# Kernel optimization log

Hardware: AMD Instinct MI355X
Metric: run time of the kernel (lower is better)

The kernel has to match this reference:

```python
import jax, jax.numpy as jnp
import numpy as np
import math

B, N, M, C, H = 4, 2048, 2048, 512, 4
D_V = C // H          # 128, used for scale and value head dim
D_QK = 2 * C // H     # 256, q/k head dim due to seq-axis split of the 2*dim qkv output
SCALE = D_V ** -0.5
EPS = 1e-12           # F.normalize eps


def _l2norm(t):
    n = jnp.linalg.norm(t, axis=-1, keepdims=True)
    return t / jnp.maximum(n, EPS)


def setup_inputs() -> dict:
    key = jax.random.key(0)
    k1, k2, k3, k4 = jax.random.split(key, 4)
    x = jax.random.normal(k1, (B, N, C), dtype=jnp.float32)
    context = jax.random.normal(k2, (B, M, C), dtype=jnp.float32)
    W_qkv = jax.random.normal(k3, (2 * C, C), dtype=jnp.float32) * 0.02  # torch Linear weight [out,in]
    W_proj = jax.random.normal(k4, (C, C), dtype=jnp.float32) * 0.02
    radius = jnp.ones((H,), dtype=jnp.float32) * math.sqrt(D_V)
    return {"x": x, "context": context, "W_qkv": W_qkv, "W_proj": W_proj, "radius": radius}


def reference(x, context, W_qkv, W_proj, radius):
    # qkv(cat([x, context], dim=1)) then split along sequence: q from x rows, k from context rows
    q = jnp.einsum('bnc,oc->bno', x, W_qkv)        # [B,N,2C]
    k = jnp.einsum('bmc,oc->bmo', context, W_qkv)  # [B,M,2C]
    q = q.reshape(B, N, H, D_QK).transpose(0, 2, 1, 3)       # [B,H,N,256]
    k = k.reshape(B, M, H, D_QK).transpose(0, 2, 1, 3)       # [B,H,M,256]
    v = context.reshape(B, M, H, D_V).transpose(0, 2, 1, 3)  # [B,H,M,128]
    r = radius[None, :, None, None]
    q = _l2norm(q) * r
    k = _l2norm(k) * r
    attn = jnp.einsum('bhnd,bhmd->bhnm', q, k) * SCALE
    attn = jax.nn.softmax(attn, axis=-1)
    out = jnp.einsum('bhnm,bhmd->bhnd', attn, v)
    out = out.transpose(0, 2, 1, 3).reshape(B, N, C)
    return jnp.einsum('bnc,oc->bno', out, W_proj)
```

## Files before the change

### kernel.cpp

```cpp
#include <hip/hip_runtime.h>
#include <hip/hip_bf16.h>
#include <stdint.h>

#define SCALE_F 0.08838834764831845f

typedef __attribute__((ext_vector_type(8))) short short8;
typedef __attribute__((ext_vector_type(4))) float f32x4;
typedef __attribute__((ext_vector_type(16))) float f32x16;

__device__ __forceinline__ void g2l16(const void* g, void* l) {
  __builtin_amdgcn_global_load_lds(
      (const __attribute__((address_space(1))) void*)g,
      (__attribute__((address_space(3))) void*)l, 16, 0, 0);
}

__global__ __launch_bounds__(256) void convert_all(
    const float* __restrict__ x, const float* __restrict__ ctx,
    const float* __restrict__ wqkv, const float* __restrict__ wproj,
    __hip_bfloat16* __restrict__ ab, __hip_bfloat16* __restrict__ wb,
    __hip_bfloat16* __restrict__ wpb)
{
  size_t qi = (size_t)blockIdx.x * 256 + threadIdx.x;
  const float* src; __hip_bfloat16* dst; size_t off;
  if (qi < 1048576)      { src = x;     dst = ab;           off = qi; }
  else if (qi < 2097152) { src = ctx;   dst = ab + 4194304; off = qi - 1048576; }
  else if (qi < 2228224) { src = wqkv;  dst = wb;           off = qi - 2097152; }
  else                   { src = wproj; dst = wpb;          off = qi - 2228224; }
  float4 v = ((const float4*)src)[off];
  union { __hip_bfloat16 h4[4]; uint2 u; } o;
  o.h4[0] = __float2bfloat16(v.x); o.h4[1] = __float2bfloat16(v.y);
  o.h4[2] = __float2bfloat16(v.z); o.h4[3] = __float2bfloat16(v.w);
  ((uint2*)dst)[off] = o.u;
}

__global__ __launch_bounds__(256) void transpose_v(
    const float* __restrict__ ctx, __hip_bfloat16* __restrict__ vt)
{
  __shared__ float tile[128][33];
  const int bid = blockIdx.x;
  const int mt = bid & 63;
  const int bh = bid >> 6;
  const int h = bh & 3, b = bh >> 2;
  const int tid = threadIdx.x;
  for (int i = 0; i < 16; ++i) {
    int idx = i * 256 + tid;
    int mm = idx >> 7, d = idx & 127;
    tile[d][mm] = ctx[((size_t)b * 2048 + mt * 32 + mm) * 512 + h * 128 + d];
  }
  __syncthreads();
  for (int i = 0; i < 16; ++i) {
    int idx = i * 256 + tid;
    int d = idx >> 5, mm = idx & 31;
    vt[((size_t)bh * 128 + d) * 2048 + mt * 32 + mm] = __float2bfloat16(tile[d][mm]);
  }
}

__global__ __launch_bounds__(256) void gemm_nt(
    const __hip_bfloat16* __restrict__ A, const __hip_bfloat16* __restrict__ B,
    float* __restrict__ C, int O, int K, int tiles_o)
{
  __shared__ __hip_bfloat16 sA[128 * 32];
  __shared__ __hip_bfloat16 sB[128 * 32];
  const int tid = threadIdx.x;
  const int wave = tid >> 6, lane = tid & 63;
  const int ln = lane & 15, q = lane >> 4;
  const int br = (blockIdx.x / tiles_o) * 128;
  const int bo = (blockIdx.x % tiles_o) * 128;
  const int wr = (wave >> 1) * 64, wc = (wave & 1) * 64;
  const __hip_bfloat16* Ab = A + (size_t)br * K;
  const __hip_bfloat16* Bb = B + (size_t)bo * K;
  const int row0 = tid >> 2, p0 = tid & 3;
  f32x4 acc[4][4] = {};
  for (int k0 = 0; k0 < K; k0 += 32) {
    for (int i = 0; i < 2; ++i) {
      int row = i * 64 + row0;
      g2l16(Ab + (size_t)row * K + k0 + p0 * 8, (char*)sA + (i * 256 + tid) * 16);
      g2l16(Bb + (size_t)row * K + k0 + p0 * 8, (char*)sB + (i * 256 + tid) * 16);
    }
    __syncthreads();
    short8 af[4], bfr[4];
    for (int mi = 0; mi < 4; ++mi)
      af[mi] = *(const short8*)(sA + (wr + mi * 16 + ln) * 32 + q * 8);
    for (int ni = 0; ni < 4; ++ni)
      bfr[ni] = *(const short8*)(sB + (wc + ni * 16 + ln) * 32 + q * 8);
    for (int mi = 0; mi < 4; ++mi)
      for (int ni = 0; ni < 4; ++ni)
        acc[mi][ni] = __builtin_amdgcn_mfma_f32_16x16x32_bf16(af[mi], bfr[ni], acc[mi][ni], 0, 0, 0);
    __syncthreads();
  }
  for (int mi = 0; mi < 4; ++mi)
    for (int ni = 0; ni < 4; ++ni) {
      int rg = br + wr + mi * 16 + q * 4;
      int cg = bo + wc + ni * 16 + ln;
      for (int r = 0; r < 4; ++r)
        C[(size_t)(rg + r) * O + cg] = acc[mi][ni][r];
    }
}

__global__ __launch_bounds__(256) void normalize_qk(
    const float* __restrict__ proj, const float* __restrict__ radius,
    __hip_bfloat16* __restrict__ qn, __hip_bfloat16* __restrict__ kn)
{
  const int r = blockIdx.x;
  const int h = threadIdx.x >> 6, lane = threadIdx.x & 63;
  float4 v = *(const float4*)(proj + (size_t)r * 1024 + h * 256 + lane * 4);
  float ss = v.x * v.x + v.y * v.y + v.z * v.z + v.w * v.w;
  for (int off = 1; off < 64; off <<= 1) ss += __shfl_xor(ss, off);
  float nrm = fmaxf(sqrtf(ss), 1e-12f);
  const bool isq = r < 8192;
  const int rr = isq ? r : r - 8192;
  const float rad = radius[h];
  const float sc = (isq ? rad * rad * SCALE_F : 1.0f) / nrm;
  __hip_bfloat16* dst = (isq ? qn : kn) +
      ((size_t)((rr >> 11) * 4 + h) * 2048 + (rr & 2047)) * 256 + lane * 4;
  union { __hip_bfloat16 h4[4]; uint2 u; } o;
  o.h4[0] = __float2bfloat16(v.x * sc);
  o.h4[1] = __float2bfloat16(v.y * sc);
  o.h4[2] = __float2bfloat16(v.z * sc);
  o.h4[3] = __float2bfloat16(v.w * sc);
  *(uint2*)dst = o.u;
}

__global__ __launch_bounds__(256, 2) void attn(
    const __hip_bfloat16* __restrict__ qn,
    const __hip_bfloat16* __restrict__ kn,
    const __hip_bfloat16* __restrict__ vt,
    float* __restrict__ Op,
    float* __restrict__ den)
{
  __shared__ __hip_bfloat16 sK[2][32 * 256];
  __shared__ __hip_bfloat16 sV[2][128 * 32];
  __shared__ __hip_bfloat16 sP[4][32 * 40];
  const int tid = threadIdx.x, wave = tid >> 6, lane = tid & 63;
  const int m32 = lane & 31, hi = lane >> 5;
  const int i = blockIdx.x;
  const int bh = (i & 7) + 8 * ((i >> 3) & 1);
  const int half = (i >> 4) & 1;
  const int nt = i >> 5;
  const int mbase = half * 1024;
  const __hip_bfloat16* Q = qn + ((size_t)bh * 2048 + nt * 128 + wave * 32) * 256;
  const __hip_bfloat16* Kp = kn + (size_t)bh * 2048 * 256;
  const __hip_bfloat16* Vp = vt + (size_t)bh * 128 * 2048;

  short8 qf[16];
  for (int kk = 0; kk < 16; ++kk)
    qf[kk] = *(const short8*)(Q + m32 * 256 + kk * 16 + hi * 8);

  f32x16 oacc[4];
  float denom[16];
  for (int v = 0; v < 4; ++v)
    for (int j = 0; j < 16; ++j) oacc[v][j] = 0.f;
  for (int j = 0; j < 16; ++j) denom[j] = 0.f;
  __hip_bfloat16* sPw = sP[wave];

  for (int t = 0; t < 4; ++t) {
    int D = t * 256 + tid, row = D >> 5, cc = D & 31;
    g2l16(Kp + (size_t)(mbase + row) * 256 + ((cc ^ (row & 7)) << 3),
          (char*)sK[0] + D * 16);
  }
  for (int t = 0; t < 2; ++t) {
    int D = t * 256 + tid, rd = D >> 2, cc = D & 3;
    g2l16(Vp + (size_t)rd * 2048 + mbase + ((cc ^ ((rd >> 1) & 3)) << 3),
          (char*)sV[0] + D * 16);
  }
  __syncthreads();

  for (int it = 0; it < 32; ++it) {
    const int cur = it & 1, nxt = cur ^ 1;
    if (it + 1 < 32) {
      const int m1 = mbase + (it + 1) * 32;
      for (int t = 0; t < 4; ++t) {
        int D = t * 256 + tid, row = D >> 5, cc = D & 31;
        g2l16(Kp + (size_t)(m1 + row) * 256 + ((cc ^ (row & 7)) << 3),
              (char*)sK[nxt] + D * 16);
      }
      for (int t = 0; t < 2; ++t) {
        int D = t * 256 + tid, rd = D >> 2, cc = D & 3;
        g2l16(Vp + (size_t)rd * 2048 + m1 + ((cc ^ ((rd >> 1) & 3)) << 3),
              (char*)sV[nxt] + D * 16);
      }
    }
    const __hip_bfloat16* sKc = sK[cur];
    f32x16 sa, sb;
    for (int j = 0; j < 16; ++j) { sa[j] = 0.f; sb[j] = 0.f; }
    for (int kk = 0; kk < 8; ++kk) {
      int ca = kk * 2 + hi, cb = (kk + 8) * 2 + hi;
      short8 kfa = *(const short8*)(sKc + m32 * 256 + ((ca ^ (m32 & 7)) << 3));
      short8 kfb = *(const short8*)(sKc + m32 * 256 + ((cb ^ (m32 & 7)) << 3));
      sa = __builtin_amdgcn_mfma_f32_32x32x16_bf16(qf[kk], kfa, sa, 0, 0, 0);
      sb = __builtin_amdgcn_mfma_f32_32x32x16_bf16(qf[kk + 8], kfb, sb, 0, 0, 0);
    }
    for (int reg = 0; reg < 16; ++reg) {
      float e = __expf(sa[reg] + sb[reg]);
      denom[reg] += e;
      int row = (reg & 3) + 8 * (reg >> 2) + 4 * hi;
      sPw[row * 40 + m32] = __float2bfloat16(e);
    }
    asm volatile("s_waitcnt lgkmcnt(0)" ::: "memory");
    const __hip_bfloat16* sVc = sV[cur];
    for (int kc = 0; kc < 2; ++kc) {
      short8 pf = *(const short8*)(sPw + m32 * 40 + kc * 16 + hi * 8);
      for (int vi = 0; vi < 4; ++vi) {
        int rd = vi * 32 + m32;
        int c = kc * 2 + hi;
        short8 vf = *(const short8*)(sVc + rd * 32 + ((c ^ ((rd >> 1) & 3)) << 3));
        oacc[vi] = __builtin_amdgcn_mfma_f32_32x32x16_bf16(pf, vf, oacc[vi], 0, 0, 0);
      }
    }
    __syncthreads();
  }

  for (int reg = 0; reg < 16; ++reg)
    for (int off = 1; off < 32; off <<= 1)
      denom[reg] += __shfl_xor(denom[reg], off);

  float* Opb = Op + ((size_t)(half * 16 + bh) * 2048) * 128;
  float* denb = den + (size_t)(half * 16 + bh) * 2048;
  const int rbase = nt * 128 + wave * 32;
  for (int vi = 0; vi < 4; ++vi)
    for (int reg = 0; reg < 16; ++reg) {
      int row = rbase + (reg & 3) + 8 * (reg >> 2) + 4 * hi;
      Opb[(size_t)row * 128 + vi * 32 + m32] = oacc[vi][reg];
    }
  if (m32 == 0)
    for (int reg = 0; reg < 16; ++reg)
      denb[rbase + (reg & 3) + 8 * (reg >> 2) + 4 * hi] = denom[reg];
}

__global__ __launch_bounds__(256) void combine(
    const float* __restrict__ Op, const float* __restrict__ den,
    __hip_bfloat16* __restrict__ ob)
{
  int qi = blockIdx.x * 256 + threadIdx.x;
  int r = qi >> 5, dq = qi & 5 * 6 + 1;
  dq = qi & 31;
  int bh = r >> 11, n = r & 2047, b = bh >> 2, h = bh & 3;
  float4 o0 = ((const float4*)Op)[qi];
  float4 o1 = ((const float4*)(Op + 4194304))[qi];
  float inv = 1.0f / (den[r] + den[32768 + r]);
  union { __hip_bfloat16 h4[4]; uint2 u; } o;
  o.h4[0] = __float2bfloat16((o0.x + o1.x) * inv);
  o.h4[1] = __float2bfloat16((o0.y + o1.y) * inv);
  o.h4[2] = __float2bfloat16((o0.z + o1.z) * inv);
  o.h4[3] = __float2bfloat16((o0.w + o1.w) * inv);
  *(uint2*)&ob[((size_t)b * 2048 + n) * 512 + h * 128 + dq * 4] = o.u;
}

extern "C" void kernel_launch(void* const* d_in, const int* in_sizes, int n_in,
                              void* d_out, int out_size, void* d_ws, size_t ws_size,
                              hipStream_t stream) {
  const float* x      = (const float*)d_in[0];
  const float* ctx    = (const float*)d_in[1];
  const float* wqkv   = (const float*)d_in[2];
  const float* wproj  = (const float*)d_in[3];
  const float* radius = (const float*)d_in[4];
  char* ws = (char*)d_ws;
  __hip_bfloat16* ab  = (__hip_bfloat16*)(ws);
  __hip_bfloat16* wb  = (__hip_bfloat16*)(ws + 16777216);
  __hip_bfloat16* wpb = (__hip_bfloat16*)(ws + 17825792);
  float*          proj= (float*)(ws + 18350080);
  float*          Op  = proj;
  float*          den = (float*)(ws + 18350080 + 33554432);
  __hip_bfloat16* qn  = (__hip_bfloat16*)(ws + 85458944);
  __hip_bfloat16* kn  = (__hip_bfloat16*)(ws + 102236160);
  __hip_bfloat16* vt  = (__hip_bfloat16*)(ws + 119013376);
  __hip_bfloat16* ob  = (__hip_bfloat16*)(ws + 127401984);
  float* out = (float*)d_out;

  convert_all<<<8960, 256, 0, stream>>>(x, ctx, wqkv, wproj, ab, wb, wpb);
  transpose_v<<<1024, 256, 0, stream>>>(ctx, vt);
  gemm_nt<<<1024, 256, 0, stream>>>(ab, wb, proj, 1024, 512, 8);
  normalize_qk<<<16384, 256, 0, stream>>>(proj, radius, qn, kn);
  attn<<<512, 256, 0, stream>>>(qn, kn, vt, Op, den);
  combine<<<4096, 256, 0, stream>>>(Op, den, ob);
  gemm_nt<<<256, 256, 0, stream>>>(ob, wpb, out, 512, 512, 4);
}
```

Before: 228.6 us.

## Transpose attention MFMAs so P stays in registers via permlane32 swap

Swaps the MFMA operand order so the score tile comes out transposed, letting the softmax probabilities be packed to bf16 and rearranged with permlane32_swap into the A-operand layout for the PV MFMA. This removes the per-iteration LDS round trip for P along with its wait, and shrinks the denominator to a single scalar per lane. The epilogue now stages the transposed output through reused sK shared memory before storing, since the accumulator layout is now transposed. Correctness depends on the permlane register mapping matching the MFMA operand layout, and the added epilogue staging needs extra waits.

```diff
diff --git a/kernel.cpp b/kernel.cpp
--- a/kernel.cpp
+++ b/kernel.cpp
@@ -7,11 +7,18 @@
 typedef __attribute__((ext_vector_type(8))) short short8;
 typedef __attribute__((ext_vector_type(4))) float f32x4;
 typedef __attribute__((ext_vector_type(16))) float f32x16;
+typedef __attribute__((ext_vector_type(2))) unsigned int uint2v;
 
 __device__ __forceinline__ void g2l16(const void* g, void* l) {
   __builtin_amdgcn_global_load_lds(
       (const __attribute__((address_space(1))) void*)g,
       (__attribute__((address_space(3))) void*)l, 16, 0, 0);
+}
+
+__device__ __forceinline__ unsigned pkbf(float a, float b) {
+  union { __hip_bfloat16 h[2]; unsigned u; } o;
+  o.h[0] = __float2bfloat16(a); o.h[1] = __float2bfloat16(b);
+  return o.u;
 }
 
 __global__ __launch_bounds__(256) void convert_all(
@@ -130,7 +137,6 @@
 {
   __shared__ __hip_bfloat16 sK[2][32 * 256];
   __shared__ __hip_bfloat16 sV[2][128 * 32];
-  __shared__ __hip_bfloat16 sP[4][32 * 40];
   const int tid = threadIdx.x, wave = tid >> 6, lane = tid & 63;
   const int m32 = lane & 31, hi = lane >> 5;
   const int i = blockIdx.x;
@@ -147,11 +153,9 @@
     qf[kk] = *(const short8*)(Q + m32 * 256 + kk * 16 + hi * 8);
 
   f32x16 oacc[4];
-  float denom[16];
   for (int v = 0; v < 4; ++v)
     for (int j = 0; j < 16; ++j) oacc[v][j] = 0.f;
-  for (int j = 0; j < 16; ++j) denom[j] = 0.f;
-  __hip_bfloat16* sPw = sP[wave];
+  float denom = 0.f;
 
   for (int t = 0; t < 4; ++t) {
     int D = t * 256 + tid, row = D >> 5, cc = D & 31;
@@ -183,48 +187,64 @@
     const __hip_bfloat16* sKc = sK[cur];
     f32x16 sa, sb;
     for (int j = 0; j < 16; ++j) { sa[j] = 0.f; sb[j] = 0.f; }
+#pragma unroll
     for (int kk = 0; kk < 8; ++kk) {
       int ca = kk * 2 + hi, cb = (kk + 8) * 2 + hi;
       short8 kfa = *(const short8*)(sKc + m32 * 256 + ((ca ^ (m32 & 7)) << 3));
       short8 kfb = *(const short8*)(sKc + m32 * 256 + ((cb ^ (m32 & 7)) << 3));
-      sa = __builtin_amdgcn_mfma_f32_32x32x16_bf16(qf[kk], kfa, sa, 0, 0, 0);
-      sb = __builtin_amdgcn_mfma_f32_32x32x16_bf16(qf[kk + 8], kfb, sb, 0, 0, 0);
-    }
+      sa = __builtin_amdgcn_mfma_f32_32x32x16_bf16(kfa, qf[kk], sa, 0, 0, 0);
+      sb = __builtin_amdgcn_mfma_f32_32x32x16_bf16(kfb, qf[kk + 8], sb, 0, 0, 0);
+    }
+    float p_[16];
+#pragma unroll
     for (int reg = 0; reg < 16; ++reg) {
       float e = __expf(sa[reg] + sb[reg]);
-      denom[reg] += e;
-      int row = (reg & 3) + 8 * (reg >> 2) + 4 * hi;
-      sPw[row * 40 + m32] = __float2bfloat16(e);
-    }
-    asm volatile("s_waitcnt lgkmcnt(0)" ::: "memory");
+      denom += e;
+      p_[reg] = e;
+    }
+    uint2v s0 = __builtin_amdgcn_permlane32_swap(pkbf(p_[0], p_[1]),  pkbf(p_[4],  p_[5]),  false, false);
+    uint2v s1 = __builtin_amdgcn_permlane32_swap(pkbf(p_[2], p_[3]),  pkbf(p_[6],  p_[7]),  false, false);
+    uint2v s2 = __builtin_amdgcn_permlane32_swap(pkbf(p_[8], p_[9]),  pkbf(p_[12], p_[13]), false, false);
+    uint2v s3 = __builtin_amdgcn_permlane32_swap(pkbf(p_[10], p_[11]), pkbf(p_[14], p_[15]), false, false);
+    union { unsigned u[4]; short8 s; } ua, ub;
+    ua.u[0] = s0.x; ua.u[1] = s1.x; ua.u[2] = s0.y; ua.u[3] = s1.y;
+    ub.u[0] = s2.x; ub.u[1] = s3.x; ub.u[2] = s2.y; ub.u[3] = s3.y;
     const __hip_bfloat16* sVc = sV[cur];
+#pragma unroll
     for (int kc = 0; kc < 2; ++kc) {
-      short8 pf = *(const short8*)(sPw + m32 * 40 + kc * 16 + hi * 8);
+      short8 pf = kc ? ub.s : ua.s;
+#pragma unroll
       for (int vi = 0; vi < 4; ++vi) {
         int rd = vi * 32 + m32;
         int c = kc * 2 + hi;
         short8 vf = *(const short8*)(sVc + rd * 32 + ((c ^ ((rd >> 1) & 3)) << 3));
-        oacc[vi] = __builtin_amdgcn_mfma_f32_32x32x16_bf16(pf, vf, oacc[vi], 0, 0, 0);
+        oacc[vi] = __builtin_amdgcn_mfma_f32_32x32x16_bf16(vf, pf, oacc[vi], 0, 0, 0);
       }
     }
     __syncthreads();
   }
 
-  for (int reg = 0; reg < 16; ++reg)
-    for (int off = 1; off < 32; off <<= 1)
-      denom[reg] += __shfl_xor(denom[reg], off);
-
-  float* Opb = Op + ((size_t)(half * 16 + bh) * 2048) * 128;
+  float dfull = denom + __shfl_xor(denom, 32);
+  float* Opb = Op + (size_t)(half * 16 + bh) * 2048 * 128;
   float* denb = den + (size_t)(half * 16 + bh) * 2048;
   const int rbase = nt * 128 + wave * 32;
-  for (int vi = 0; vi < 4; ++vi)
+  if (hi == 0) denb[rbase + m32] = dfull;
+  float* sc_ = (float*)(&sK[0][0]) + wave * 1056;
+#pragma unroll
+  for (int vi = 0; vi < 4; ++vi) {
+#pragma unroll
     for (int reg = 0; reg < 16; ++reg) {
-      int row = rbase + (reg & 3) + 8 * (reg >> 2) + 4 * hi;
-      Opb[(size_t)row * 128 + vi * 32 + m32] = oacc[vi][reg];
-    }
-  if (m32 == 0)
-    for (int reg = 0; reg < 16; ++reg)
-      denb[rbase + (reg & 3) + 8 * (reg >> 2) + 4 * hi] = denom[reg];
+      int dL = (reg & 3) + 8 * (reg >> 2) + 4 * hi;
+      sc_[m32 * 33 + dL] = oacc[vi][reg];
+    }
+    asm volatile("s_waitcnt lgkmcnt(0)" ::: "memory");
+#pragma unroll
+    for (int qq = 0; qq < 16; ++qq) {
+      int qr = qq * 2 + hi;
+      Opb[(size_t)(rbase + qr) * 128 + vi * 32 + m32] = sc_[qr * 33 + m32];
+    }
+    asm volatile("s_waitcnt lgkmcnt(0)" ::: "memory");
+  }
 }
 
 __global__ __launch_bounds__(256) void combine(
@@ -232,8 +252,8 @@
     __hip_bfloat16* __restrict__ ob)
 {
   int qi = blockIdx.x * 256 + threadIdx.x;
-  int r = qi >> 5, dq = qi & 5 * 6 + 1;
-  dq = qi & 31;
+  int r = qi >> 5;
+  int dq = qi & 31;
   int bh = r >> 11, n = r & 2047, b = bh >> 2, h = bh & 3;
   float4 o0 = ((const float4*)Op)[qi];
   float4 o1 = ((const float4*)(Op + 4194304))[qi];
```

Measured after the change: 223.1 us. -2.4%, faster.
